# Kernel tuning notes

Measured on AMD Instinct MI355X. Metric: run time of the kernel, lower is better.

Reference implementation:

```python
import jax, jax.numpy as jnp
import numpy as np

# anchor encoding indices: [x,y,z,log w,log l,log h,sin,cos,vx,vy,vz]
NUM_HEADS = 8
LN_EPS = 1e-5


def layer_norm(x, g, b):
    mu = jnp.mean(x, axis=-1, keepdims=True)
    var = jnp.var(x, axis=-1, keepdims=True)
    return (x - mu) * jax.lax.rsqrt(var + LN_EPS) * g + b


def align_anchors_to_frame(anchor, Tm):
    # anchor: (..., N, 11), Tm: (..., 4, 4)
    R = Tm[..., :3, :3]
    t = Tm[..., :3, 3]
    center = jnp.einsum('...ij,...nj->...ni', R, anchor[..., 0:3]) + t[..., None, :]
    size = anchor[..., 3:6]
    yaw = jnp.einsum('...ij,...nj->...ni', R[..., :2, :2], anchor[..., 6:8])
    vel = jnp.einsum('...ij,...nj->...ni', R, anchor[..., 8:11])
    return jnp.concatenate([center, size, yaw, vel], axis=-1)


def setup_inputs() -> dict:
    key = jax.random.key(0)
    ks = jax.random.split(key, 12)
    B, T, N, C, E, A = 2, 12, 1024, 256, 256, 11
    inp = {
        'seq_features': jax.random.normal(ks[0], (B, T, N, C), jnp.float32),
        'seq_anchors': jax.random.normal(ks[1], (B, T, N, A), jnp.float32),
        'T_ego_his2cur': jax.random.normal(ks[2], (B, T, 4, 4), jnp.float32),
        'Wf': jax.random.normal(ks[3], (E, C), jnp.float32) * (C ** -0.5),
        'bf': jnp.zeros((E,), jnp.float32),
        'Wa': jax.random.normal(ks[4], (E, A), jnp.float32) * (A ** -0.5),
        'ba': jnp.zeros((E,), jnp.float32),
        'Win': jax.random.normal(ks[5], (3 * E, E), jnp.float32) * (E ** -0.5),
        'bin_': jnp.zeros((3 * E,), jnp.float32),
        'gamma': jnp.ones((E,), jnp.float32),
        'beta': jnp.zeros((E,), jnp.float32),
    }
    return inp


def reference(seq_features, seq_anchors, T_ego_his2cur, Wf, bf, Wa, ba, Win, bin_, gamma, beta):
    B, T, N, C = seq_features.shape
    E = gamma.shape[0]
    H = NUM_HEADS
    D = E // H

    feat_cur = seq_features[:, 1:]    # (B,T-1,N,C)
    feat_prev = seq_features[:, :-1]
    anc_cur = seq_anchors[:, 1:]
    anc_prev = align_anchors_to_frame(seq_anchors[:, :-1], T_ego_his2cur[:, 1:])

    tok_cur = layer_norm(feat_cur @ Wf.T + bf + anc_cur @ Wa.T + ba, gamma, beta)
    tok_prev = layer_norm(feat_prev @ Wf.T + bf + anc_prev @ Wa.T + ba, gamma, beta)

    Wq, Wk = Win[:E], Win[E:2 * E]
    bq, bk = bin_[:E], bin_[E:2 * E]
    scale = np.float32(D) ** np.float32(-0.5)
    q = ((tok_cur @ Wq.T + bq) * scale).reshape(B, T - 1, N, H, D)
    k = (tok_prev @ Wk.T + bk).reshape(B, T - 1, N, H, D)

    scores = jnp.einsum('btnhd,btmhd->bthnm', q, k)  # (B,T-1,H,N,N)
    attn = jax.nn.softmax(scores, axis=-1).mean(axis=2)  # head-averaged weights

    eye = jnp.broadcast_to(jnp.eye(N, dtype=seq_features.dtype), (B, 1, N, N))
    return jnp.concatenate([eye, attn], axis=1)  # (B,T,N,N)
```

## Files before the change

kernel.cpp:

```cpp
#include <hip/hip_runtime.h>
#include <hip/hip_bf16.h>
#include <math.h>

#define LN_EPS 1e-5f

typedef short bf16x8 __attribute__((ext_vector_type(8)));
typedef float f32x4 __attribute__((ext_vector_type(4)));

__device__ inline short f2bf(float f) {
  union { float f; unsigned u; } v; v.f = f;
  unsigned r = v.u + 0x7FFFu + ((v.u >> 16) & 1u);
  return (short)(r >> 16);
}
__device__ inline float bf2f(unsigned short s) {
  union { unsigned u; float f; } v; v.u = ((unsigned)s) << 16;
  return v.f;
}
__device__ inline float fast_exp2(float x) {
#if __has_builtin(__builtin_amdgcn_exp2f)
  return __builtin_amdgcn_exp2f(x);
#else
  return __expf(x * 0.69314718056f);
#endif
}

__global__ __launch_bounds__(256) void gemm_feat(const float* __restrict__ Ap,
    const float* __restrict__ W, const float* __restrict__ bias,
    short* __restrict__ Out)
{
  __shared__ short lda[64][40];
  __shared__ short ldb[64][40];
  const int tid = threadIdx.x;
  const int bm = blockIdx.x * 64, bn = blockIdx.y * 64;
  const int wid = tid >> 6, lane = tid & 63;
  const int quad = lane >> 4, l15 = lane & 15;
  const int wm = (wid & 1) * 32, wn = (wid >> 1) * 32;
  const int srow = tid >> 2, sseg = tid & 3;

  f32x4 z = {0.f, 0.f, 0.f, 0.f};
  f32x4 acc[2][2];
  acc[0][0] = z; acc[0][1] = z; acc[1][0] = z; acc[1][1] = z;

  for (int kk = 0; kk < 256; kk += 32) {
    {
      const float* ap = Ap + (size_t)(bm + srow) * 256 + kk + sseg * 8;
      f32x4 x0 = *(const f32x4*)ap;
      f32x4 x1 = *(const f32x4*)(ap + 4);
      bf16x8 vv;
      vv[0] = f2bf(x0[0]); vv[1] = f2bf(x0[1]); vv[2] = f2bf(x0[2]); vv[3] = f2bf(x0[3]);
      vv[4] = f2bf(x1[0]); vv[5] = f2bf(x1[1]); vv[6] = f2bf(x1[2]); vv[7] = f2bf(x1[3]);
      *(bf16x8*)&lda[srow][sseg * 8] = vv;
    }
    {
      const float* wp = W + (size_t)(bn + srow) * 256 + kk + sseg * 8;
      f32x4 x0 = *(const f32x4*)wp;
      f32x4 x1 = *(const f32x4*)(wp + 4);
      bf16x8 vv;
      vv[0] = f2bf(x0[0]); vv[1] = f2bf(x0[1]); vv[2] = f2bf(x0[2]); vv[3] = f2bf(x0[3]);
      vv[4] = f2bf(x1[0]); vv[5] = f2bf(x1[1]); vv[6] = f2bf(x1[2]); vv[7] = f2bf(x1[3]);
      *(bf16x8*)&ldb[srow][sseg * 8] = vv;
    }
    __syncthreads();
    bf16x8 af0 = *(const bf16x8*)&lda[wm + l15][quad * 8];
    bf16x8 af1 = *(const bf16x8*)&lda[wm + 16 + l15][quad * 8];
    bf16x8 bq0 = *(const bf16x8*)&ldb[wn + l15][quad * 8];
    bf16x8 bq1 = *(const bf16x8*)&ldb[wn + 16 + l15][quad * 8];
    acc[0][0] = __builtin_amdgcn_mfma_f32_16x16x32_bf16(af0, bq0, acc[0][0], 0, 0, 0);
    acc[0][1] = __builtin_amdgcn_mfma_f32_16x16x32_bf16(af0, bq1, acc[0][1], 0, 0, 0);
    acc[1][0] = __builtin_amdgcn_mfma_f32_16x16x32_bf16(af1, bq0, acc[1][0], 0, 0, 0);
    acc[1][1] = __builtin_amdgcn_mfma_f32_16x16x32_bf16(af1, bq1, acc[1][1], 0, 0, 0);
    __syncthreads();
  }

  #pragma unroll
  for (int i = 0; i < 2; ++i)
    #pragma unroll
    for (int j = 0; j < 2; ++j)
      #pragma unroll
      for (int r = 0; r < 4; ++r) {
        int grow = bm + wm + i * 16 + quad * 4 + r;
        int gcol = bn + wn + j * 16 + l15;
        Out[(size_t)grow * 256 + gcol] = f2bf(acc[i][j][r] + bias[gcol]);
      }
}

__global__ __launch_bounds__(256) void gemm_qk(const short* __restrict__ tokc,
    const short* __restrict__ tokp, const float* __restrict__ Win,
    const float* __restrict__ binv, short* __restrict__ qb, short* __restrict__ kb)
{
  const int sel = blockIdx.z;
  const short* Ap = sel ? tokp : tokc;
  const float* W = Win + (size_t)sel * 65536;
  const float* bias = binv + sel * 256;
  const float alpha = sel ? 1.0f : 0.17677669529663687f * 1.4426950408889634f;
  short* Out = sel ? kb : qb;

  __shared__ short lda[64][40];
  __shared__ short ldb[64][40];
  const int tid = threadIdx.x;
  const int bm = blockIdx.x * 64, bn = blockIdx.y * 64;
  const int wid = tid >> 6, lane = tid & 63;
  const int quad = lane >> 4, l15 = lane & 15;
  const int wm = (wid & 1) * 32, wn = (wid >> 1) * 32;
  const int srow = tid >> 2, sseg = tid & 3;

  f32x4 z = {0.f, 0.f, 0.f, 0.f};
  f32x4 acc[2][2];
  acc[0][0] = z; acc[0][1] = z; acc[1][0] = z; acc[1][1] = z;

  for (int kk = 0; kk < 256; kk += 32) {
    *(bf16x8*)&lda[srow][sseg * 8] =
        *(const bf16x8*)(Ap + (size_t)(bm + srow) * 256 + kk + sseg * 8);
    {
      const float* wp = W + (size_t)(bn + srow) * 256 + kk + sseg * 8;
      f32x4 x0 = *(const f32x4*)wp;
      f32x4 x1 = *(const f32x4*)(wp + 4);
      bf16x8 vv;
      vv[0] = f2bf(x0[0]); vv[1] = f2bf(x0[1]); vv[2] = f2bf(x0[2]); vv[3] = f2bf(x0[3]);
      vv[4] = f2bf(x1[0]); vv[5] = f2bf(x1[1]); vv[6] = f2bf(x1[2]); vv[7] = f2bf(x1[3]);
      *(bf16x8*)&ldb[srow][sseg * 8] = vv;
    }
    __syncthreads();
    bf16x8 af0 = *(const bf16x8*)&lda[wm + l15][quad * 8];
    bf16x8 af1 = *(const bf16x8*)&lda[wm + 16 + l15][quad * 8];
    bf16x8 bq0 = *(const bf16x8*)&ldb[wn + l15][quad * 8];
    bf16x8 bq1 = *(const bf16x8*)&ldb[wn + 16 + l15][quad * 8];
    acc[0][0] = __builtin_amdgcn_mfma_f32_16x16x32_bf16(af0, bq0, acc[0][0], 0, 0, 0);
    acc[0][1] = __builtin_amdgcn_mfma_f32_16x16x32_bf16(af0, bq1, acc[0][1], 0, 0, 0);
    acc[1][0] = __builtin_amdgcn_mfma_f32_16x16x32_bf16(af1, bq0, acc[1][0], 0, 0, 0);
    acc[1][1] = __builtin_amdgcn_mfma_f32_16x16x32_bf16(af1, bq1, acc[1][1], 0, 0, 0);
    __syncthreads();
  }

  #pragma unroll
  for (int i = 0; i < 2; ++i)
    #pragma unroll
    for (int j = 0; j < 2; ++j)
      #pragma unroll
      for (int r = 0; r < 4; ++r) {
        int grow = bm + wm + i * 16 + quad * 4 + r;
        int gcol = bn + wn + j * 16 + l15;
        float v = (acc[i][j][r] + bias[gcol]) * alpha;
        int btr = grow >> 10, nn = grow & 1023, h = gcol >> 5, d = gcol & 31;
        Out[(((size_t)btr * 8 + h) * 1024 + nn) * 32 + d] = f2bf(v);
      }
}

__global__ __launch_bounds__(256) void anchor_ln(const short* __restrict__ featproj,
  const float* __restrict__ anchors, const float* __restrict__ Tego,
  const float* __restrict__ Wa, const float* __restrict__ ba,
  const float* __restrict__ gamma, const float* __restrict__ beta,
  short* __restrict__ tok_cur, short* __restrict__ tok_prev)
{
  const int wid = threadIdx.x >> 6, lane = threadIdx.x & 63;
  const int tok = blockIdx.x * 4 + wid;
  const int which = tok >= 22528 ? 1 : 0;
  const int rem = tok - which * 22528;
  const int bt = rem >> 10;
  const int n = rem & 1023;
  const int b = bt / 11, t = bt - b * 11;
  const int tt = which ? t : t + 1;

  const float* ap = anchors + (((size_t)b * 12 + tt) * 1024 + n) * 11;
  float a[11];
  #pragma unroll
  for (int j = 0; j < 11; ++j) a[j] = ap[j];
  if (which) {
    const float* Tm = Tego + ((size_t)b * 12 + t + 1) * 16;
    float r00 = Tm[0], r01 = Tm[1], r02 = Tm[2],  t0 = Tm[3];
    float r10 = Tm[4], r11 = Tm[5], r12 = Tm[6],  t1 = Tm[7];
    float r20 = Tm[8], r21 = Tm[9], r22 = Tm[10], t2 = Tm[11];
    float a0 = a[0], a1 = a[1], a2 = a[2];
    float a6 = a[6], a7 = a[7], a8 = a[8], a9 = a[9], a10 = a[10];
    a[0] = r00 * a0 + r01 * a1 + r02 * a2 + t0;
    a[1] = r10 * a0 + r11 * a1 + r12 * a2 + t1;
    a[2] = r20 * a0 + r21 * a1 + r22 * a2 + t2;
    a[6] = r00 * a6 + r01 * a7;
    a[7] = r10 * a6 + r11 * a7;
    a[8] = r00 * a8 + r01 * a9 + r02 * a10;
    a[9] = r10 * a8 + r11 * a9 + r12 * a10;
    a[10] = r20 * a8 + r21 * a9 + r22 * a10;
  }

  const int c0 = lane * 4;
  const size_t frow = (((size_t)b * 12 + tt) * 1024 + n) * 256 + c0;
  ushort4 raw = *(const ushort4*)(featproj + frow);
  f32x4 bav = *(const f32x4*)(ba + c0);
  float v[4];
  v[0] = bf2f(raw.x) + bav[0]; v[1] = bf2f(raw.y) + bav[1];
  v[2] = bf2f(raw.z) + bav[2]; v[3] = bf2f(raw.w) + bav[3];
  #pragma unroll
  for (int c = 0; c < 4; ++c) {
    const float* war = Wa + (size_t)(c0 + c) * 11;
    float acc = 0.f;
    #pragma unroll
    for (int j = 0; j < 11; ++j) acc += war[j] * a[j];
    v[c] += acc;
  }
  float s1 = v[0] + v[1] + v[2] + v[3];
  float s2 = v[0]*v[0] + v[1]*v[1] + v[2]*v[2] + v[3]*v[3];
  #pragma unroll
  for (int off = 1; off < 64; off <<= 1) { s1 += __shfl_xor(s1, off); s2 += __shfl_xor(s2, off); }
  float mean = s1 * (1.0f / 256.0f);
  float var = s2 * (1.0f / 256.0f) - mean * mean;
  float rstd = rsqrtf(var + LN_EPS);
  f32x4 gv = *(const f32x4*)(gamma + c0);
  f32x4 bv = *(const f32x4*)(beta + c0);
  ushort4 o;
  o.x = (unsigned short)f2bf((v[0] - mean) * rstd * gv[0] + bv[0]);
  o.y = (unsigned short)f2bf((v[1] - mean) * rstd * gv[1] + bv[1]);
  o.z = (unsigned short)f2bf((v[2] - mean) * rstd * gv[2] + bv[2]);
  o.w = (unsigned short)f2bf((v[3] - mean) * rstd * gv[3] + bv[3]);
  short* dst = which ? tok_prev : tok_cur;
  *(ushort4*)(dst + ((size_t)bt * 1024 + n) * 256 + c0) = o;
}

__global__ __launch_bounds__(256) void denom_kernel(const short* __restrict__ q,
  const short* __restrict__ k, float* __restrict__ dinv)
{
  __shared__ short kst[2][4096];
  const int tid = threadIdx.x, wid = tid >> 6, lane = tid & 63;
  const int quad = lane >> 4, l15 = lane & 15;
  const int h = blockIdx.y, bt = blockIdx.z;
  const int n0 = blockIdx.x * 64 + wid * 16;
  const size_t base = ((size_t)bt * 8 + h) * 1024 * 32;
  bf16x8 qf = *(const bf16x8*)(q + base + (size_t)(n0 + l15) * 32 + quad * 8);
  const short* ksA = k + base + (size_t)(wid * 16) * 32 + lane * 8;
  const short* ksB = k + base + (size_t)((wid + 4) * 16) * 32 + lane * 8;
  short* lwA = &kst[0][wid * 512 + lane * 8];
  short* lwB = &kst[0][(wid + 4) * 512 + lane * 8];

  f32x4 z = {0.f, 0.f, 0.f, 0.f};
  float sum0 = 0, sum1 = 0, sum2 = 0, sum3 = 0;

  bf16x8 stA = *(const bf16x8*)ksA;
  bf16x8 stB = *(const bf16x8*)ksB;

  #pragma unroll 1
  for (int rd = 0; rd < 8; ++rd) {
    const int buf = rd & 1;
    *(bf16x8*)(lwA + buf * 4096) = stA;
    *(bf16x8*)(lwB + buf * 4096) = stB;
    __syncthreads();
    if (rd < 7) {
      stA = *(const bf16x8*)(ksA + (size_t)(rd + 1) * 128 * 32);
      stB = *(const bf16x8*)(ksB + (size_t)(rd + 1) * 128 * 32);
    }
    #pragma unroll
    for (int s = 0; s < 8; ++s) {
      bf16x8 kf = *(const bf16x8*)&kst[buf][s * 512 + l15 * 32 + quad * 8];
      f32x4 sc = __builtin_amdgcn_mfma_f32_16x16x32_bf16(qf, kf, z, 0, 0, 0);
      sum0 += fast_exp2(sc[0]); sum1 += fast_exp2(sc[1]);
      sum2 += fast_exp2(sc[2]); sum3 += fast_exp2(sc[3]);
    }
    __syncthreads();
  }
  #pragma unroll
  for (int off = 1; off < 16; off <<= 1) {
    sum0 += __shfl_xor(sum0, off); sum1 += __shfl_xor(sum1, off);
    sum2 += __shfl_xor(sum2, off); sum3 += __shfl_xor(sum3, off);
  }
  if (l15 == 0) {
    float* dp = dinv + ((size_t)bt * 8 + h) * 1024 + n0 + quad * 4;
    dp[0] = 1.f / sum0; dp[1] = 1.f / sum1; dp[2] = 1.f / sum2; dp[3] = 1.f / sum3;
  }
}

__global__ __launch_bounds__(256) void prob_kernel(const short* __restrict__ q,
  const short* __restrict__ k, const float* __restrict__ dinv, float* __restrict__ out)
{
  __shared__ short kst[2][4096];
  const int tid = threadIdx.x, wid = tid >> 6, lane = tid & 63;
  const int quad = lane >> 4, l15 = lane & 15;
  const int bt = blockIdx.z;
  const int n0 = blockIdx.x * 64 + wid * 16;
  const int mbase = blockIdx.y * 128;
  const int b = bt / 11, t = bt - b * 11;
  bf16x8 qf[8];
  float invd[8][4];
  #pragma unroll
  for (int h = 0; h < 8; ++h) {
    const size_t base = ((size_t)bt * 8 + h) * 1024 * 32;
    qf[h] = *(const bf16x8*)(q + base + (size_t)(n0 + l15) * 32 + quad * 8);
    const float* dp = dinv + ((size_t)bt * 8 + h) * 1024 + n0 + quad * 4;
    #pragma unroll
    for (int r = 0; r < 4; ++r) invd[h][r] = dp[r] * 0.125f;
  }
  const short* ksA = k + (((size_t)bt * 8 + wid    ) * 1024 + mbase) * 32 + lane * 8;
  const short* ksB = k + (((size_t)bt * 8 + wid + 4) * 1024 + mbase) * 32 + lane * 8;
  short* lwA = &kst[0][wid * 512 + lane * 8];
  short* lwB = &kst[0][(wid + 4) * 512 + lane * 8];

  float* ob = out + ((size_t)(b * 12 + t + 1)) * 1024 * 1024
                  + (size_t)(n0 + quad * 4) * 1024 + l15;
  f32x4 z = {0.f, 0.f, 0.f, 0.f};

  bf16x8 stA = *(const bf16x8*)ksA;
  bf16x8 stB = *(const bf16x8*)ksB;

  #pragma unroll 1
  for (int mt = 0; mt < 8; ++mt) {
    const int buf = mt & 1;
    *(bf16x8*)(lwA + buf * 4096) = stA;
    *(bf16x8*)(lwB + buf * 4096) = stB;
    __syncthreads();
    if (mt < 7) {
      stA = *(const bf16x8*)(ksA + (size_t)(mt + 1) * 16 * 32);
      stB = *(const bf16x8*)(ksB + (size_t)(mt + 1) * 16 * 32);
    }
    float P0 = 0, P1 = 0, P2 = 0, P3 = 0;
    #pragma unroll
    for (int h = 0; h < 8; ++h) {
      bf16x8 kf = *(const bf16x8*)&kst[buf][h * 512 + l15 * 32 + quad * 8];
      f32x4 s = __builtin_amdgcn_mfma_f32_16x16x32_bf16(qf[h], kf, z, 0, 0, 0);
      P0 += fast_exp2(s[0]) * invd[h][0];
      P1 += fast_exp2(s[1]) * invd[h][1];
      P2 += fast_exp2(s[2]) * invd[h][2];
      P3 += fast_exp2(s[3]) * invd[h][3];
    }
    float* op = ob + mbase + mt * 16;
    op[0] = P0; op[1024] = P1; op[2048] = P2; op[3072] = P3;
    __syncthreads();
  }
}

__global__ __launch_bounds__(256) void eye_kernel(float* __restrict__ out) {
  int gid = blockIdx.x * 256 + threadIdx.x;
  int b = gid >> 18, rem = gid & 262143;
  int n = rem >> 8, m4 = rem & 255;
  f32x4 v = {0.f, 0.f, 0.f, 0.f};
  int c = n - m4 * 4;
  if (c >= 0 && c < 4) v[c] = 1.0f;
  *(f32x4*)(out + (size_t)b * 12582912 + (size_t)n * 1024 + m4 * 4) = v;
}

extern "C" void kernel_launch(void* const* d_in, const int* in_sizes, int n_in,
                              void* d_out, int out_size, void* d_ws, size_t ws_size,
                              hipStream_t stream)
{
  const float* sf   = (const float*)d_in[0];
  const float* sa   = (const float*)d_in[1];
  const float* te   = (const float*)d_in[2];
  const float* Wf   = (const float*)d_in[3];
  const float* bfv  = (const float*)d_in[4];
  const float* Wa   = (const float*)d_in[5];
  const float* ba   = (const float*)d_in[6];
  const float* Win  = (const float*)d_in[7];
  const float* binv = (const float*)d_in[8];
  const float* gam  = (const float*)d_in[9];
  const float* bet  = (const float*)d_in[10];
  float* out = (float*)d_out;

  char* w = (char*)d_ws;
  short* featproj = (short*)w;  w += 12582912;
  short* tok_cur  = (short*)w;  w += 11534336;
  short* tok_prev = (short*)w;  w += 11534336;
  short* qb       = (short*)w;  w += 11534336;
  short* kb       = (short*)w;  w += 11534336;
  float* dinv     = (float*)w;  w += 720896;

  gemm_feat<<<dim3(384, 4), 256, 0, stream>>>(sf, Wf, bfv, featproj);
  anchor_ln<<<dim3(11264), 256, 0, stream>>>(featproj, sa, te, Wa, ba, gam, bet, tok_cur, tok_prev);
  gemm_qk<<<dim3(352, 4, 2), 256, 0, stream>>>(tok_cur, tok_prev, Win, binv, qb, kb);
  denom_kernel<<<dim3(16, 8, 22), 256, 0, stream>>>(qb, kb, dinv);
  prob_kernel<<<dim3(16, 8, 22), 256, 0, stream>>>(qb, kb, dinv, out);
  eye_kernel<<<dim3(2048), 256, 0, stream>>>(out);
}
```

Before: 262.9 us.

## Swizzle K tiles in LDS, reorder double buffer, and double query rows per wave in denom

Each wave in the denominator kernel now handles 32 query rows instead of 16, so every K fragment read from LDS feeds two MFMAs, and the grid is halved. In both attention kernels the K tile is written to LDS with an XOR swizzle to avoid bank conflicts on the fragment reads. The next buffer is now written after the compute, which drops one barrier per iteration. The cost is more registers per thread in the denominator kernel and fewer blocks there.

```diff
diff --git a/kernel.cpp b/kernel.cpp
--- a/kernel.cpp
+++ b/kernel.cpp
@@ -222,47 +222,66 @@
   const int tid = threadIdx.x, wid = tid >> 6, lane = tid & 63;
   const int quad = lane >> 4, l15 = lane & 15;
   const int h = blockIdx.y, bt = blockIdx.z;
-  const int n0 = blockIdx.x * 64 + wid * 16;
+  const int n0 = blockIdx.x * 128 + wid * 32;
   const size_t base = ((size_t)bt * 8 + h) * 1024 * 32;
-  bf16x8 qf = *(const bf16x8*)(q + base + (size_t)(n0 + l15) * 32 + quad * 8);
+  bf16x8 qf0 = *(const bf16x8*)(q + base + (size_t)(n0 + l15) * 32 + quad * 8);
+  bf16x8 qf1 = *(const bf16x8*)(q + base + (size_t)(n0 + 16 + l15) * 32 + quad * 8);
   const short* ksA = k + base + (size_t)(wid * 16) * 32 + lane * 8;
   const short* ksB = k + base + (size_t)((wid + 4) * 16) * 32 + lane * 8;
-  short* lwA = &kst[0][wid * 512 + lane * 8];
-  short* lwB = &kst[0][(wid + 4) * 512 + lane * 8];
+  const int wswz = ((lane & 3) ^ ((lane >> 3) & 3)) * 8;
+  const int rswz = (quad ^ ((l15 >> 1) & 3)) * 8;
+  short* lwA = &kst[0][wid * 512 + (lane >> 2) * 32 + wswz];
+  short* lwB = &kst[0][(wid + 4) * 512 + (lane >> 2) * 32 + wswz];
 
   f32x4 z = {0.f, 0.f, 0.f, 0.f};
-  float sum0 = 0, sum1 = 0, sum2 = 0, sum3 = 0;
+  float sum0[4] = {0.f, 0.f, 0.f, 0.f};
+  float sum1[4] = {0.f, 0.f, 0.f, 0.f};
 
   bf16x8 stA = *(const bf16x8*)ksA;
   bf16x8 stB = *(const bf16x8*)ksB;
+  *(bf16x8*)lwA = stA;
+  *(bf16x8*)lwB = stB;
+  __syncthreads();
 
   #pragma unroll 1
   for (int rd = 0; rd < 8; ++rd) {
     const int buf = rd & 1;
-    *(bf16x8*)(lwA + buf * 4096) = stA;
-    *(bf16x8*)(lwB + buf * 4096) = stB;
-    __syncthreads();
     if (rd < 7) {
       stA = *(const bf16x8*)(ksA + (size_t)(rd + 1) * 128 * 32);
       stB = *(const bf16x8*)(ksB + (size_t)(rd + 1) * 128 * 32);
     }
     #pragma unroll
     for (int s = 0; s < 8; ++s) {
-      bf16x8 kf = *(const bf16x8*)&kst[buf][s * 512 + l15 * 32 + quad * 8];
-      f32x4 sc = __builtin_amdgcn_mfma_f32_16x16x32_bf16(qf, kf, z, 0, 0, 0);
-      sum0 += fast_exp2(sc[0]); sum1 += fast_exp2(sc[1]);
-      sum2 += fast_exp2(sc[2]); sum3 += fast_exp2(sc[3]);
+      bf16x8 kf = *(const bf16x8*)&kst[buf][s * 512 + l15 * 32 + rswz];
+      f32x4 sc0 = __builtin_amdgcn_mfma_f32_16x16x32_bf16(qf0, kf, z, 0, 0, 0);
+      f32x4 sc1 = __builtin_amdgcn_mfma_f32_16x16x32_bf16(qf1, kf, z, 0, 0, 0);
+      #pragma unroll
+      for (int r = 0; r < 4; ++r) {
+        sum0[r] += fast_exp2(sc0[r]);
+        sum1[r] += fast_exp2(sc1[r]);
+      }
+    }
+    if (rd < 7) {
+      *(bf16x8*)(lwA + ((buf ^ 1) << 12)) = stA;
+      *(bf16x8*)(lwB + ((buf ^ 1) << 12)) = stB;
     }
     __syncthreads();
   }
   #pragma unroll
   for (int off = 1; off < 16; off <<= 1) {
-    sum0 += __shfl_xor(sum0, off); sum1 += __shfl_xor(sum1, off);
-    sum2 += __shfl_xor(sum2, off); sum3 += __shfl_xor(sum3, off);
+    #pragma unroll
+    for (int r = 0; r < 4; ++r) {
+      sum0[r] += __shfl_xor(sum0[r], off);
+      sum1[r] += __shfl_xor(sum1[r], off);
+    }
   }
   if (l15 == 0) {
     float* dp = dinv + ((size_t)bt * 8 + h) * 1024 + n0 + quad * 4;
-    dp[0] = 1.f / sum0; dp[1] = 1.f / sum1; dp[2] = 1.f / sum2; dp[3] = 1.f / sum3;
+    #pragma unroll
+    for (int r = 0; r < 4; ++r) {
+      dp[r] = 1.f / sum0[r];
+      dp[16 + r] = 1.f / sum1[r];
+    }
   }
 }
 
@@ -288,8 +307,10 @@
   }
   const short* ksA = k + (((size_t)bt * 8 + wid    ) * 1024 + mbase) * 32 + lane * 8;
   const short* ksB = k + (((size_t)bt * 8 + wid + 4) * 1024 + mbase) * 32 + lane * 8;
-  short* lwA = &kst[0][wid * 512 + lane * 8];
-  short* lwB = &kst[0][(wid + 4) * 512 + lane * 8];
+  const int wswz = ((lane & 3) ^ ((lane >> 3) & 3)) * 8;
+  const int rswz = (quad ^ ((l15 >> 1) & 3)) * 8;
+  short* lwA = &kst[0][wid * 512 + (lane >> 2) * 32 + wswz];
+  short* lwB = &kst[0][(wid + 4) * 512 + (lane >> 2) * 32 + wswz];
 
   float* ob = out + ((size_t)(b * 12 + t + 1)) * 1024 * 1024
                   + (size_t)(n0 + quad * 4) * 1024 + l15;
@@ -297,13 +318,13 @@
 
   bf16x8 stA = *(const bf16x8*)ksA;
   bf16x8 stB = *(const bf16x8*)ksB;
+  *(bf16x8*)lwA = stA;
+  *(bf16x8*)lwB = stB;
+  __syncthreads();
 
   #pragma unroll 1
   for (int mt = 0; mt < 8; ++mt) {
     const int buf = mt & 1;
-    *(bf16x8*)(lwA + buf * 4096) = stA;
-    *(bf16x8*)(lwB + buf * 4096) = stB;
-    __syncthreads();
     if (mt < 7) {
       stA = *(const bf16x8*)(ksA + (size_t)(mt + 1) * 16 * 32);
       stB = *(const bf16x8*)(ksB + (size_t)(mt + 1) * 16 * 32);
@@ -311,7 +332,7 @@
     float P0 = 0, P1 = 0, P2 = 0, P3 = 0;
     #pragma unroll
     for (int h = 0; h < 8; ++h) {
-      bf16x8 kf = *(const bf16x8*)&kst[buf][h * 512 + l15 * 32 + quad * 8];
+      bf16x8 kf = *(const bf16x8*)&kst[buf][h * 512 + l15 * 32 + rswz];
       f32x4 s = __builtin_amdgcn_mfma_f32_16x16x32_bf16(qf[h], kf, z, 0, 0, 0);
       P0 += fast_exp2(s[0]) * invd[h][0];
       P1 += fast_exp2(s[1]) * invd[h][1];
@@ -320,6 +341,10 @@
     }
     float* op = ob + mbase + mt * 16;
     op[0] = P0; op[1024] = P1; op[2048] = P2; op[3072] = P3;
+    if (mt < 7) {
+      *(bf16x8*)(lwA + ((buf ^ 1) << 12)) = stA;
+      *(bf16x8*)(lwB + ((buf ^ 1) << 12)) = stB;
+    }
     __syncthreads();
   }
 }
@@ -362,7 +387,7 @@
   gemm_feat<<<dim3(384, 4), 256, 0, stream>>>(sf, Wf, bfv, featproj);
   anchor_ln<<<dim3(11264), 256, 0, stream>>>(featproj, sa, te, Wa, ba, gam, bet, tok_cur, tok_prev);
   gemm_qk<<<dim3(352, 4, 2), 256, 0, stream>>>(tok_cur, tok_prev, Win, binv, qb, kb);
-  denom_kernel<<<dim3(16, 8, 22), 256, 0, stream>>>(qb, kb, dinv);
+  denom_kernel<<<dim3(8, 8, 22), 256, 0, stream>>>(qb, kb, dinv);
   prob_kernel<<<dim3(16, 8, 22), 256, 0, stream>>>(qb, kb, dinv, out);
   eye_kernel<<<dim3(2048), 256, 0, stream>>>(out);
 }
```

Measured after the change: 268.0 us. About the same (+1.9%).

## Pre-convert inputs to bf16, drop LDS staging, swap MFMA operands for row-contiguous stores

Applied to the files above, without the earlier changes.

Adds a conversion kernel that casts seq_features, Wf and the q/k part of Win to bf16 once, so the GEMMs load bf16 directly instead of converting in every tile. The denominator and probability kernels stop staging K through LDS double buffers and read K fragments straight from global/L2, removing the block barriers. The MFMA operands are swapped so each lane holds four consecutive m columns, which lets the probability kernel write float4 rows instead of strided scalar stores. The extra conversion pass adds an additional read/write of the feature tensor and one more launch.

```diff
diff --git a/kernel.cpp b/kernel.cpp
--- a/kernel.cpp
+++ b/kernel.cpp
@@ -24,8 +24,26 @@
 #endif
 }
 
-__global__ __launch_bounds__(256) void gemm_feat(const float* __restrict__ Ap,
-    const float* __restrict__ W, const float* __restrict__ bias,
+__global__ __launch_bounds__(256) void convert_kernel(const float* __restrict__ sf,
+    const float* __restrict__ Wf, const float* __restrict__ Win,
+    short* __restrict__ sfb, short* __restrict__ Wfb, short* __restrict__ Wqkb)
+{
+  size_t i = ((size_t)blockIdx.x * 256 + threadIdx.x) * 8;
+  const float* src;
+  short* dst;
+  if (i < 6291456) { src = sf + i; dst = sfb + i; }
+  else if (i < 6356992) { src = Wf + (i - 6291456); dst = Wfb + (i - 6291456); }
+  else { src = Win + (i - 6356992); dst = Wqkb + (i - 6356992); }
+  f32x4 x0 = *(const f32x4*)src;
+  f32x4 x1 = *(const f32x4*)(src + 4);
+  bf16x8 v;
+  v[0] = f2bf(x0[0]); v[1] = f2bf(x0[1]); v[2] = f2bf(x0[2]); v[3] = f2bf(x0[3]);
+  v[4] = f2bf(x1[0]); v[5] = f2bf(x1[1]); v[6] = f2bf(x1[2]); v[7] = f2bf(x1[3]);
+  *(bf16x8*)dst = v;
+}
+
+__global__ __launch_bounds__(256) void gemm_feat(const short* __restrict__ Ap,
+    const short* __restrict__ W, const float* __restrict__ bias,
     short* __restrict__ Out)
 {
   __shared__ short lda[64][40];
@@ -42,24 +60,10 @@
   acc[0][0] = z; acc[0][1] = z; acc[1][0] = z; acc[1][1] = z;
 
   for (int kk = 0; kk < 256; kk += 32) {
-    {
-      const float* ap = Ap + (size_t)(bm + srow) * 256 + kk + sseg * 8;
-      f32x4 x0 = *(const f32x4*)ap;
-      f32x4 x1 = *(const f32x4*)(ap + 4);
-      bf16x8 vv;
-      vv[0] = f2bf(x0[0]); vv[1] = f2bf(x0[1]); vv[2] = f2bf(x0[2]); vv[3] = f2bf(x0[3]);
-      vv[4] = f2bf(x1[0]); vv[5] = f2bf(x1[1]); vv[6] = f2bf(x1[2]); vv[7] = f2bf(x1[3]);
-      *(bf16x8*)&lda[srow][sseg * 8] = vv;
-    }
-    {
-      const float* wp = W + (size_t)(bn + srow) * 256 + kk + sseg * 8;
-      f32x4 x0 = *(const f32x4*)wp;
-      f32x4 x1 = *(const f32x4*)(wp + 4);
-      bf16x8 vv;
-      vv[0] = f2bf(x0[0]); vv[1] = f2bf(x0[1]); vv[2] = f2bf(x0[2]); vv[3] = f2bf(x0[3]);
-      vv[4] = f2bf(x1[0]); vv[5] = f2bf(x1[1]); vv[6] = f2bf(x1[2]); vv[7] = f2bf(x1[3]);
-      *(bf16x8*)&ldb[srow][sseg * 8] = vv;
-    }
+    *(bf16x8*)&lda[srow][sseg * 8] =
+        *(const bf16x8*)(Ap + (size_t)(bm + srow) * 256 + kk + sseg * 8);
+    *(bf16x8*)&ldb[srow][sseg * 8] =
+        *(const bf16x8*)(W + (size_t)(bn + srow) * 256 + kk + sseg * 8);
     __syncthreads();
     bf16x8 af0 = *(const bf16x8*)&lda[wm + l15][quad * 8];
     bf16x8 af1 = *(const bf16x8*)&lda[wm + 16 + l15][quad * 8];
@@ -85,12 +89,12 @@
 }
 
 __global__ __launch_bounds__(256) void gemm_qk(const short* __restrict__ tokc,
-    const short* __restrict__ tokp, const float* __restrict__ Win,
+    const short* __restrict__ tokp, const short* __restrict__ Wqkb,
     const float* __restrict__ binv, short* __restrict__ qb, short* __restrict__ kb)
 {
   const int sel = blockIdx.z;
   const short* Ap = sel ? tokp : tokc;
-  const float* W = Win + (size_t)sel * 65536;
+  const short* W = Wqkb + (size_t)sel * 65536;
   const float* bias = binv + sel * 256;
   const float alpha = sel ? 1.0f : 0.17677669529663687f * 1.4426950408889634f;
   short* Out = sel ? kb : qb;
@@ -111,15 +115,8 @@
   for (int kk = 0; kk < 256; kk += 32) {
     *(bf16x8*)&lda[srow][sseg * 8] =
         *(const bf16x8*)(Ap + (size_t)(bm + srow) * 256 + kk + sseg * 8);
-    {
-      const float* wp = W + (size_t)(bn + srow) * 256 + kk + sseg * 8;
-      f32x4 x0 = *(const f32x4*)wp;
-      f32x4 x1 = *(const f32x4*)(wp + 4);
-      bf16x8 vv;
-      vv[0] = f2bf(x0[0]); vv[1] = f2bf(x0[1]); vv[2] = f2bf(x0[2]); vv[3] = f2bf(x0[3]);
-      vv[4] = f2bf(x1[0]); vv[5] = f2bf(x1[1]); vv[6] = f2bf(x1[2]); vv[7] = f2bf(x1[3]);
-      *(bf16x8*)&ldb[srow][sseg * 8] = vv;
-    }
+    *(bf16x8*)&ldb[srow][sseg * 8] =
+        *(const bf16x8*)(W + (size_t)(bn + srow) * 256 + kk + sseg * 8);
     __syncthreads();
     bf16x8 af0 = *(const bf16x8*)&lda[wm + l15][quad * 8];
     bf16x8 af1 = *(const bf16x8*)&lda[wm + 16 + l15][quad * 8];
@@ -218,109 +215,65 @@
 __global__ __launch_bounds__(256) void denom_kernel(const short* __restrict__ q,
   const short* __restrict__ k, float* __restrict__ dinv)
 {
-  __shared__ short kst[2][4096];
   const int tid = threadIdx.x, wid = tid >> 6, lane = tid & 63;
   const int quad = lane >> 4, l15 = lane & 15;
   const int h = blockIdx.y, bt = blockIdx.z;
   const int n0 = blockIdx.x * 64 + wid * 16;
-  const size_t base = ((size_t)bt * 8 + h) * 1024 * 32;
+  const size_t base = ((size_t)bt * 8 + h) * 32768;
   bf16x8 qf = *(const bf16x8*)(q + base + (size_t)(n0 + l15) * 32 + quad * 8);
-  const short* ksA = k + base + (size_t)(wid * 16) * 32 + lane * 8;
-  const short* ksB = k + base + (size_t)((wid + 4) * 16) * 32 + lane * 8;
-  short* lwA = &kst[0][wid * 512 + lane * 8];
-  short* lwB = &kst[0][(wid + 4) * 512 + lane * 8];
+  const short* kp = k + base + l15 * 32 + quad * 8;
 
   f32x4 z = {0.f, 0.f, 0.f, 0.f};
-  float sum0 = 0, sum1 = 0, sum2 = 0, sum3 = 0;
-
-  bf16x8 stA = *(const bf16x8*)ksA;
-  bf16x8 stB = *(const bf16x8*)ksB;
-
-  #pragma unroll 1
-  for (int rd = 0; rd < 8; ++rd) {
-    const int buf = rd & 1;
-    *(bf16x8*)(lwA + buf * 4096) = stA;
-    *(bf16x8*)(lwB + buf * 4096) = stB;
-    __syncthreads();
-    if (rd < 7) {
-      stA = *(const bf16x8*)(ksA + (size_t)(rd + 1) * 128 * 32);
-      stB = *(const bf16x8*)(ksB + (size_t)(rd + 1) * 128 * 32);
-    }
-    #pragma unroll
-    for (int s = 0; s < 8; ++s) {
-      bf16x8 kf = *(const bf16x8*)&kst[buf][s * 512 + l15 * 32 + quad * 8];
-      f32x4 sc = __builtin_amdgcn_mfma_f32_16x16x32_bf16(qf, kf, z, 0, 0, 0);
-      sum0 += fast_exp2(sc[0]); sum1 += fast_exp2(sc[1]);
-      sum2 += fast_exp2(sc[2]); sum3 += fast_exp2(sc[3]);
-    }
-    __syncthreads();
-  }
-  #pragma unroll
-  for (int off = 1; off < 16; off <<= 1) {
-    sum0 += __shfl_xor(sum0, off); sum1 += __shfl_xor(sum1, off);
-    sum2 += __shfl_xor(sum2, off); sum3 += __shfl_xor(sum3, off);
-  }
-  if (l15 == 0) {
-    float* dp = dinv + ((size_t)bt * 8 + h) * 1024 + n0 + quad * 4;
-    dp[0] = 1.f / sum0; dp[1] = 1.f / sum1; dp[2] = 1.f / sum2; dp[3] = 1.f / sum3;
-  }
+  float s0 = 0.f, s1 = 0.f, s2 = 0.f, s3 = 0.f;
+  #pragma unroll 8
+  for (int mt = 0; mt < 64; ++mt) {
+    bf16x8 kf = *(const bf16x8*)(kp + mt * 512);
+    f32x4 sc = __builtin_amdgcn_mfma_f32_16x16x32_bf16(kf, qf, z, 0, 0, 0);
+    s0 += fast_exp2(sc[0]); s1 += fast_exp2(sc[1]);
+    s2 += fast_exp2(sc[2]); s3 += fast_exp2(sc[3]);
+  }
+  float s = (s0 + s1) + (s2 + s3);
+  s += __shfl_xor(s, 16);
+  s += __shfl_xor(s, 32);
+  if (quad == 0)
+    dinv[((size_t)bt * 8 + h) * 1024 + n0 + l15] = 1.f / s;
 }
 
 __global__ __launch_bounds__(256) void prob_kernel(const short* __restrict__ q,
   const short* __restrict__ k, const float* __restrict__ dinv, float* __restrict__ out)
 {
-  __shared__ short kst[2][4096];
   const int tid = threadIdx.x, wid = tid >> 6, lane = tid & 63;
   const int quad = lane >> 4, l15 = lane & 15;
   const int bt = blockIdx.z;
-  const int n0 = blockIdx.x * 64 + wid * 16;
+  const int n = blockIdx.x * 64 + wid * 16 + l15;
   const int mbase = blockIdx.y * 128;
   const int b = bt / 11, t = bt - b * 11;
+
   bf16x8 qf[8];
-  float invd[8][4];
+  float invd[8];
   #pragma unroll
   for (int h = 0; h < 8; ++h) {
-    const size_t base = ((size_t)bt * 8 + h) * 1024 * 32;
-    qf[h] = *(const bf16x8*)(q + base + (size_t)(n0 + l15) * 32 + quad * 8);
-    const float* dp = dinv + ((size_t)bt * 8 + h) * 1024 + n0 + quad * 4;
-    #pragma unroll
-    for (int r = 0; r < 4; ++r) invd[h][r] = dp[r] * 0.125f;
-  }
-  const short* ksA = k + (((size_t)bt * 8 + wid    ) * 1024 + mbase) * 32 + lane * 8;
-  const short* ksB = k + (((size_t)bt * 8 + wid + 4) * 1024 + mbase) * 32 + lane * 8;
-  short* lwA = &kst[0][wid * 512 + lane * 8];
-  short* lwB = &kst[0][(wid + 4) * 512 + lane * 8];
-
-  float* ob = out + ((size_t)(b * 12 + t + 1)) * 1024 * 1024
-                  + (size_t)(n0 + quad * 4) * 1024 + l15;
+    const size_t base = ((size_t)bt * 8 + h) * 32768;
+    qf[h] = *(const bf16x8*)(q + base + (size_t)n * 32 + quad * 8);
+    invd[h] = dinv[((size_t)bt * 8 + h) * 1024 + n] * 0.125f;
+  }
+  const short* kp = k + (size_t)bt * 262144 + (size_t)(mbase + l15) * 32 + quad * 8;
+  float* ob = out + ((size_t)(b * 12 + t + 1) * 1024 + n) * 1024 + mbase + quad * 4;
   f32x4 z = {0.f, 0.f, 0.f, 0.f};
 
-  bf16x8 stA = *(const bf16x8*)ksA;
-  bf16x8 stB = *(const bf16x8*)ksB;
-
-  #pragma unroll 1
+  #pragma unroll 2
   for (int mt = 0; mt < 8; ++mt) {
-    const int buf = mt & 1;
-    *(bf16x8*)(lwA + buf * 4096) = stA;
-    *(bf16x8*)(lwB + buf * 4096) = stB;
-    __syncthreads();
-    if (mt < 7) {
-      stA = *(const bf16x8*)(ksA + (size_t)(mt + 1) * 16 * 32);
-      stB = *(const bf16x8*)(ksB + (size_t)(mt + 1) * 16 * 32);
-    }
-    float P0 = 0, P1 = 0, P2 = 0, P3 = 0;
+    f32x4 p = z;
     #pragma unroll
     for (int h = 0; h < 8; ++h) {
-      bf16x8 kf = *(const bf16x8*)&kst[buf][h * 512 + l15 * 32 + quad * 8];
-      f32x4 s = __builtin_amdgcn_mfma_f32_16x16x32_bf16(qf[h], kf, z, 0, 0, 0);
-      P0 += fast_exp2(s[0]) * invd[h][0];
-      P1 += fast_exp2(s[1]) * invd[h][1];
-      P2 += fast_exp2(s[2]) * invd[h][2];
-      P3 += fast_exp2(s[3]) * invd[h][3];
+      bf16x8 kf = *(const bf16x8*)(kp + (size_t)h * 32768 + mt * 512);
+      f32x4 s = __builtin_amdgcn_mfma_f32_16x16x32_bf16(kf, qf[h], z, 0, 0, 0);
+      p[0] += fast_exp2(s[0]) * invd[h];
+      p[1] += fast_exp2(s[1]) * invd[h];
+      p[2] += fast_exp2(s[2]) * invd[h];
+      p[3] += fast_exp2(s[3]) * invd[h];
     }
-    float* op = ob + mbase + mt * 16;
-    op[0] = P0; op[1024] = P1; op[2048] = P2; op[3072] = P3;
-    __syncthreads();
+    *(f32x4*)(ob + mt * 16) = p;
   }
 }
 
@@ -358,10 +311,14 @@
   short* qb       = (short*)w;  w += 11534336;
   short* kb       = (short*)w;  w += 11534336;
   float* dinv     = (float*)w;  w += 720896;
-
-  gemm_feat<<<dim3(384, 4), 256, 0, stream>>>(sf, Wf, bfv, featproj);
+  short* sfb      = (short*)w;  w += 12582912;
+  short* Wfb      = (short*)w;  w += 131072;
+  short* Wqkb     = (short*)w;  w += 262144;
+
+  convert_kernel<<<dim3(3168), 256, 0, stream>>>(sf, Wf, Win, sfb, Wfb, Wqkb);
+  gemm_feat<<<dim3(384, 4), 256, 0, stream>>>(sfb, Wfb, bfv, featproj);
   anchor_ln<<<dim3(11264), 256, 0, stream>>>(featproj, sa, te, Wa, ba, gam, bet, tok_cur, tok_prev);
-  gemm_qk<<<dim3(352, 4, 2), 256, 0, stream>>>(tok_cur, tok_prev, Win, binv, qb, kb);
+  gemm_qk<<<dim3(352, 4, 2), 256, 0, stream>>>(tok_cur, tok_prev, Wqkb, binv, qb, kb);
   denom_kernel<<<dim3(16, 8, 22), 256, 0, stream>>>(qb, kb, dinv);
   prob_kernel<<<dim3(16, 8, 22), 256, 0, stream>>>(qb, kb, dinv, out);
   eye_kernel<<<dim3(2048), 256, 0, stream>>>(out);
```

New measurement: 295.0 us. 1.12x slower.
